# Performance work log

Measured on AMD Instinct MI355X. Metric: run time of the kernel, lower is better.

## Reference

```python
import jax, jax.numpy as jnp
import numpy as np

IN_FEATURES = 8192
OUT_FEATURES = 8192
BATCH_TOKENS = 64
QMAX = 255  # uint8-style storage range


def setup_inputs() -> dict:
    key = jax.random.key(0)
    k_x, k_w, k_s, k_z, k_b = jax.random.split(key, 5)
    x = jax.random.normal(k_x, (BATCH_TOKENS, IN_FEATURES), dtype=jnp.float32)
    # quantized weight stored as integer codes in [0, 255], per-output-channel qparams
    qweight = jax.random.randint(k_w, (OUT_FEATURES, IN_FEATURES), 0, QMAX + 1, dtype=jnp.int32)
    scales = jax.random.uniform(k_s, (OUT_FEATURES,), dtype=jnp.float32, minval=0.001, maxval=0.02)
    zero_points = jax.random.randint(k_z, (OUT_FEATURES,), 100, 156, dtype=jnp.int32)
    bias = jax.random.normal(k_b, (OUT_FEATURES,), dtype=jnp.float32)
    return {"x": x, "qweight": qweight, "scales": scales, "zero_points": zero_points, "bias": bias}


def reference(x, qweight, scales, zero_points, bias):
    # Dequantize per-output-channel affine quantized weight: W = (q - zp) * scale
    # qweight: [out, in], scales/zero_points: [out]
    w = (qweight.astype(jnp.float32) - zero_points.astype(jnp.float32)[:, None]) * scales[:, None]
    # y = x @ W^T + b : [tokens, out]
    return jnp.einsum('ti,oi->to', x, w) + bias
```

## Files before the change

### kernel.cpp

```cpp
#include <hip/hip_runtime.h>
#include <hip/hip_fp16.h>

#define T_DIM 64
#define K_DIM 8192
#define N_DIM 8192
#define KSPLIT 16
#define KC (K_DIM / KSPLIT)
#define BN 128
#define NBX (N_DIM / BN)

typedef __fp16 half8_t __attribute__((ext_vector_type(8)));
typedef __fp16 half4_t __attribute__((ext_vector_type(4)));
typedef __fp16 half2_t __attribute__((ext_vector_type(2)));
typedef float  f32x4   __attribute__((ext_vector_type(4)));
typedef int    i32x4   __attribute__((ext_vector_type(4)));

__global__ __launch_bounds__(256) void prep_kernel(const float* __restrict__ x,
                                                   __fp16* __restrict__ xh,
                                                   float* __restrict__ rowsum_part) {
    const int t = blockIdx.x >> 2;
    const int q = blockIdx.x & 3;
    const int kbase = q * (K_DIM / 4) + threadIdx.x * 8;
    const float* xr = x + (size_t)t * K_DIM + kbase;
    __fp16* xhr = xh + (size_t)t * K_DIM + kbase;

    f32x4 v0 = *(const f32x4*)xr;
    f32x4 v1 = *(const f32x4*)(xr + 4);
    half8_t h;
    h[0] = (__fp16)v0[0]; h[1] = (__fp16)v0[1]; h[2] = (__fp16)v0[2]; h[3] = (__fp16)v0[3];
    h[4] = (__fp16)v1[0]; h[5] = (__fp16)v1[1]; h[6] = (__fp16)v1[2]; h[7] = (__fp16)v1[3];
    *(half8_t*)xhr = h;

    float s = 0.0f;
    #pragma unroll
    for (int i = 0; i < 8; ++i) s += (float)h[i];

    #pragma unroll
    for (int off = 32; off > 0; off >>= 1) s += __shfl_down(s, off, 64);
    __shared__ float red[4];
    const int lane = threadIdx.x & 63;
    const int w = threadIdx.x >> 6;
    if (lane == 0) red[w] = s;
    __syncthreads();
    if (threadIdx.x == 0) rowsum_part[t * 4 + q] = red[0] + red[1] + red[2] + red[3];
}

__global__ __launch_bounds__(256, 4) void woq_gemm_kernel(
        const int* __restrict__ qw, const __fp16* __restrict__ xh,
        float* __restrict__ part) {
    const int bx = blockIdx.x;
    const int bz = blockIdx.y;
    const int tid = threadIdx.x;
    const int wid = __builtin_amdgcn_readfirstlane(tid >> 6);
    const int lane = tid & 63;
    const int r = lane & 15;
    const int g = lane >> 4;

    const int n_wave = bx * BN + wid * 32;
    const int k0 = bz * KC;

    const __fp16* aptr = xh + (size_t)r * K_DIM + k0 + g * 8;
    const int* bptr = qw + (size_t)(n_wave + r) * K_DIM + k0 + g * 8;

    f32x4 acc[4][2] = {};

    #pragma unroll 2
    for (int kk = 0; kk < KC; kk += 32) {
        half8_t af[4];
        #pragma unroll
        for (int m = 0; m < 4; ++m)
            af[m] = *(const half8_t*)(aptr + (size_t)m * 16 * K_DIM + kk);

        half8_t bf[2];
        #pragma unroll
        for (int n = 0; n < 2; ++n) {
            const int* bp = bptr + (size_t)n * 16 * K_DIM + kk;
            i32x4 q0 = *(const i32x4*)bp;
            i32x4 q1 = *(const i32x4*)(bp + 4);
            union { half8_t h8; half2_t h2[4]; } u;
            u.h2[0] = __builtin_amdgcn_cvt_pkrtz((float)q0[0], (float)q0[1]);
            u.h2[1] = __builtin_amdgcn_cvt_pkrtz((float)q0[2], (float)q0[3]);
            u.h2[2] = __builtin_amdgcn_cvt_pkrtz((float)q1[0], (float)q1[1]);
            u.h2[3] = __builtin_amdgcn_cvt_pkrtz((float)q1[2], (float)q1[3]);
            bf[n] = u.h8;
        }

        #pragma unroll
        for (int m = 0; m < 4; ++m)
            #pragma unroll
            for (int n = 0; n < 2; ++n)
                acc[m][n] = __builtin_amdgcn_mfma_f32_16x16x32_f16(af[m], bf[n], acc[m][n], 0, 0, 0);
    }

    float* pp = part + (((size_t)bz * NBX + bx) * 4 + wid) * 2048 + g * 16 + r;
    #pragma unroll
    for (int n = 0; n < 2; ++n)
        #pragma unroll
        for (int m = 0; m < 4; ++m)
            #pragma unroll
            for (int j = 0; j < 4; ++j)
                pp[((n * 4 + m) * 4 + j) * 64] = acc[m][n][j];
}

__global__ __launch_bounds__(256) void reduce_kernel(
        const float* __restrict__ part, const float* __restrict__ rowsum_part,
        const float* __restrict__ scales, const int* __restrict__ zps,
        const float* __restrict__ bias, float* __restrict__ out) {
    const int idx = blockIdx.x * 256 + threadIdx.x;
    const int e = idx * 4;
    const int t = e >> 13;
    const int c = e & (N_DIM - 1);
    const int bx = c >> 7;
    const int wid = (c >> 5) & 3;
    const int n = (c >> 4) & 1;
    const int r0 = c & 15;
    const int m = t >> 4;
    const int g = (t >> 2) & 3;
    const int j = t & 3;

    const size_t off = ((size_t)bx * 4 + wid) * 2048 + ((n * 4 + m) * 4 + j) * 64 + g * 16 + r0;
    f32x4 s = {0.f, 0.f, 0.f, 0.f};
    #pragma unroll
    for (int bz = 0; bz < KSPLIT; ++bz)
        s += *(const f32x4*)(part + (size_t)bz * (NBX * 4 * 2048) + off);

    const float rs = rowsum_part[t * 4 + 0] + rowsum_part[t * 4 + 1] +
                     rowsum_part[t * 4 + 2] + rowsum_part[t * 4 + 3];

    f32x4 sc = *(const f32x4*)(scales + c);
    i32x4 zp = *(const i32x4*)(zps + c);
    f32x4 bv = *(const f32x4*)(bias + c);
    f32x4 y;
    #pragma unroll
    for (int i = 0; i < 4; ++i)
        y[i] = sc[i] * (s[i] - (float)zp[i] * rs) + bv[i];
    *(f32x4*)(out + e) = y;
}

extern "C" void kernel_launch(void* const* d_in, const int* in_sizes, int n_in,
                              void* d_out, int out_size, void* d_ws, size_t ws_size,
                              hipStream_t stream) {
    const float* x      = (const float*)d_in[0];
    const int*   qw     = (const int*)d_in[1];
    const float* scales = (const float*)d_in[2];
    const int*   zps    = (const int*)d_in[3];
    const float* bias   = (const float*)d_in[4];
    float* out = (float*)d_out;

    __fp16* xh          = (__fp16*)d_ws;
    float*  rowsum_part = (float*)((char*)d_ws + (size_t)T_DIM * K_DIM * sizeof(__fp16));
    float*  part        = (float*)((char*)d_ws + (2u << 20));

    prep_kernel<<<256, 256, 0, stream>>>(x, xh, rowsum_part);
    woq_gemm_kernel<<<dim3(NBX, KSPLIT), 256, 0, stream>>>(qw, xh, part);
    reduce_kernel<<<(T_DIM * N_DIM / 4) / 256, 256, 0, stream>>>(
        part, rowsum_part, scales, zps, bias, out);
}
```

Before: 389.4 us.

## Stage int32 weight tiles through LDS with async double-buffered global_load_lds

```diff
diff --git a/kernel.cpp b/kernel.cpp
--- a/kernel.cpp
+++ b/kernel.cpp
@@ -1,16 +1,16 @@
 #include <hip/hip_runtime.h>
-#include <hip/hip_fp16.h>
 
 #define T_DIM 64
 #define K_DIM 8192
 #define N_DIM 8192
-#define KSPLIT 16
+#define KSPLIT 8
 #define KC (K_DIM / KSPLIT)
 #define BN 128
 #define NBX (N_DIM / BN)
+#define BK 64
+#define NT (KC / BK)
 
 typedef __fp16 half8_t __attribute__((ext_vector_type(8)));
-typedef __fp16 half4_t __attribute__((ext_vector_type(4)));
 typedef __fp16 half2_t __attribute__((ext_vector_type(2)));
 typedef float  f32x4   __attribute__((ext_vector_type(4)));
 typedef int    i32x4   __attribute__((ext_vector_type(4)));
@@ -45,9 +45,11 @@
     if (threadIdx.x == 0) rowsum_part[t * 4 + q] = red[0] + red[1] + red[2] + red[3];
 }
 
-__global__ __launch_bounds__(256, 4) void woq_gemm_kernel(
+__global__ __launch_bounds__(256, 2) void woq_gemm_kernel(
         const int* __restrict__ qw, const __fp16* __restrict__ xh,
         float* __restrict__ part) {
+    __shared__ int ldsB[2][128 * BK];
+
     const int bx = blockIdx.x;
     const int bz = blockIdx.y;
     const int tid = threadIdx.x;
@@ -56,40 +58,68 @@
     const int r = lane & 15;
     const int g = lane >> 4;
 
-    const int n_wave = bx * BN + wid * 32;
+    const int n_base = bx * BN;
     const int k0 = bz * KC;
 
     const __fp16* aptr = xh + (size_t)r * K_DIM + k0 + g * 8;
-    const int* bptr = qw + (size_t)(n_wave + r) * K_DIM + k0 + g * 8;
 
     f32x4 acc[4][2] = {};
 
-    #pragma unroll 2
-    for (int kk = 0; kk < KC; kk += 32) {
-        half8_t af[4];
-        #pragma unroll
-        for (int m = 0; m < 4; ++m)
-            af[m] = *(const half8_t*)(aptr + (size_t)m * 16 * K_DIM + kk);
+#define STAGE(buf, kt) do {                                                       \
+        _Pragma("unroll")                                                         \
+        for (int j = 0; j < 8; ++j) {                                             \
+            const int row_t = wid * 32 + j * 4 + g;                               \
+            const int* src = qw + (size_t)(n_base + row_t) * K_DIM + k0           \
+                             + (kt) * BK + ((r ^ (row_t & 15)) << 2);             \
+            int* dst = &ldsB[buf][(wid * 32 + j * 4) * BK];                       \
+            __builtin_amdgcn_global_load_lds(                                     \
+                (const __attribute__((address_space(1))) void*)src,               \
+                (__attribute__((address_space(3))) void*)dst, 16, 0, 0);          \
+        }                                                                         \
+    } while (0)
 
-        half8_t bf[2];
-        #pragma unroll
-        for (int n = 0; n < 2; ++n) {
-            const int* bp = bptr + (size_t)n * 16 * K_DIM + kk;
-            i32x4 q0 = *(const i32x4*)bp;
-            i32x4 q1 = *(const i32x4*)(bp + 4);
-            union { half8_t h8; half2_t h2[4]; } u;
-            u.h2[0] = __builtin_amdgcn_cvt_pkrtz((float)q0[0], (float)q0[1]);
-            u.h2[1] = __builtin_amdgcn_cvt_pkrtz((float)q0[2], (float)q0[3]);
-            u.h2[2] = __builtin_amdgcn_cvt_pkrtz((float)q1[0], (float)q1[1]);
-            u.h2[3] = __builtin_amdgcn_cvt_pkrtz((float)q1[2], (float)q1[3]);
-            bf[n] = u.h8;
-        }
+#define COMPUTE(buf, kt) do {                                                     \
+        _Pragma("unroll")                                                         \
+        for (int s = 0; s < 2; ++s) {                                             \
+            half8_t af[4];                                                        \
+            _Pragma("unroll")                                                     \
+            for (int m = 0; m < 4; ++m)                                           \
+                af[m] = *(const half8_t*)(aptr + (size_t)m * 16 * K_DIM           \
+                                          + (kt) * BK + s * 32);                  \
+            half8_t bf[2];                                                        \
+            _Pragma("unroll")                                                     \
+            for (int n = 0; n < 2; ++n) {                                         \
+                const int row_t = wid * 32 + n * 16 + r;                          \
+                i32x4 q0 = *(const i32x4*)&ldsB[buf][row_t * BK                   \
+                                + (((s * 8 + g * 2 + 0) ^ r) << 2)];              \
+                i32x4 q1 = *(const i32x4*)&ldsB[buf][row_t * BK                   \
+                                + (((s * 8 + g * 2 + 1) ^ r) << 2)];              \
+                union { half8_t h8; half2_t h2[4]; } u;                           \
+                u.h2[0] = __builtin_amdgcn_cvt_pkrtz((float)q0[0], (float)q0[1]); \
+                u.h2[1] = __builtin_amdgcn_cvt_pkrtz((float)q0[2], (float)q0[3]); \
+                u.h2[2] = __builtin_amdgcn_cvt_pkrtz((float)q1[0], (float)q1[1]); \
+                u.h2[3] = __builtin_amdgcn_cvt_pkrtz((float)q1[2], (float)q1[3]); \
+                bf[n] = u.h8;                                                     \
+            }                                                                     \
+            _Pragma("unroll")                                                     \
+            for (int m = 0; m < 4; ++m)                                           \
+                _Pragma("unroll")                                                 \
+                for (int n = 0; n < 2; ++n)                                       \
+                    acc[m][n] = __builtin_amdgcn_mfma_f32_16x16x32_f16(           \
+                        af[m], bf[n], acc[m][n], 0, 0, 0);                        \
+        }                                                                         \
+    } while (0)
 
-        #pragma unroll
-        for (int m = 0; m < 4; ++m)
-            #pragma unroll
-            for (int n = 0; n < 2; ++n)
-                acc[m][n] = __builtin_amdgcn_mfma_f32_16x16x32_f16(af[m], bf[n], acc[m][n], 0, 0, 0);
+    STAGE(0, 0);
+    __syncthreads();
+
+    for (int kt = 0; kt < NT; kt += 2) {
+        if (kt + 1 < NT) STAGE(1, kt + 1);
+        COMPUTE(0, kt);
+        __syncthreads();
+        if (kt + 2 < NT) STAGE(0, kt + 2);
+        COMPUTE(1, kt + 1);
+        __syncthreads();
     }
 
     float* pp = part + (((size_t)bz * NBX + bx) * 4 + wid) * 2048 + g * 16 + r;
@@ -148,7 +178,7 @@
     float* out = (float*)d_out;
 
     __fp16* xh          = (__fp16*)d_ws;
-    float*  rowsum_part = (float*)((char*)d_ws + (size_t)T_DIM * K_DIM * sizeof(__fp16));
+    float*  rowsum_part = (float*)((char*)d_ws + (1u << 20));
     float*  part        = (float*)((char*)d_ws + (2u << 20));
 
     prep_kernel<<<256, 256, 0, stream>>>(x, xh, rowsum_part);
```

Result: slower. 426.0 us (+9.4%).
